# Optimization experiments

Measured on AMD Instinct MI355X. Metric: run time of the kernel, lower is better.

Reference implementation:

```python
import jax, jax.numpy as jnp
import numpy as np

HEADS = 4
KS = 7          # neighborhood kernel size
EPS = 1e-5
C = 64
N, H, W = 8, 64, 64


def _gather_idx(L, k):
    # NATTEN-style neighborhood: window centered at pixel, shifted to stay in bounds.
    start = jnp.clip(jnp.arange(L) - k // 2, 0, L - k)            # [L]
    idx = start[:, None] + jnp.arange(k)                           # [L, k] absolute neighbor idx
    # relative-position-bias index: (query - neighbor) + (k-1) in [0, 2k-2]
    rel = (jnp.arange(L) - start)[:, None] + (k - 1) - jnp.arange(k)[None, :]  # [L, k]
    return idx, rel


def na2d(x, qkv_w, qkv_b, rpb, proj_w, proj_b):
    # x: [N, H, W, C] -> neighborhood attention with rel-pos bias
    n, h, w, c = x.shape
    hd = c // HEADS
    scale = hd ** -0.5
    qkv = (x @ qkv_w.T + qkv_b).reshape(n, h, w, 3, HEADS, hd)
    q = qkv[..., 0, :, :] * scale                                  # [n,h,w,heads,hd]
    k = qkv[..., 1, :, :]
    v = qkv[..., 2, :, :]
    idx_h, rel_h = _gather_idx(h, KS)
    idx_w, rel_w = _gather_idx(w, KS)
    # gather neighborhoods: [n, h, k, w, k, heads, hd]
    kg = k[:, idx_h][:, :, :, idx_w]
    vg = v[:, idx_h][:, :, :, idx_w]
    attn = jnp.einsum('nijhd,niajbhd->nijhab', q, kg)              # [n,h,w,heads,k,k]
    bias = rpb[:, rel_h, :]                                        # [heads, h, k, 2k-1]
    bias = jnp.take(bias, rel_w, axis=-1)                          # [heads, h, k, w, k]
    bias = jnp.transpose(bias, (1, 3, 0, 2, 4))                    # [h, w, heads, k, k]
    attn = attn + bias
    a = jax.nn.softmax(attn.reshape(n, h, w, HEADS, KS * KS), axis=-1).reshape(attn.shape)
    out = jnp.einsum('nijhab,niajbhd->nijhd', a, vg).reshape(n, h, w, c)
    return out @ proj_w.T + proj_b


def setup_inputs() -> dict:
    key = jax.random.key(0)
    ks = jax.random.split(key, 12)
    s = 0.02
    return {
        'x': jax.random.normal(ks[0], (N, C, H, W), jnp.float32),
        'gn_w': jnp.ones((C,), jnp.float32),
        'gn_b': jnp.zeros((C,), jnp.float32),
        'qkv_w': jax.random.normal(ks[1], (3 * C, C), jnp.float32) * s,
        'qkv_b': jnp.zeros((3 * C,), jnp.float32),
        'rpb': jax.random.normal(ks[2], (HEADS, 2 * KS - 1, 2 * KS - 1), jnp.float32) * s,
        'proj_w': jax.random.normal(ks[3], (C, C), jnp.float32) * s,
        'proj_b': jnp.zeros((C,), jnp.float32),
        'ln_w': jnp.ones((C,), jnp.float32),
        'ln_b': jnp.zeros((C,), jnp.float32),
        'fc1_w': jax.random.normal(ks[4], (4 * C, C), jnp.float32) * s,
        'fc1_b': jnp.zeros((4 * C,), jnp.float32),
        'fc2_w': jax.random.normal(ks[5], (C, 4 * C), jnp.float32) * s,
        'fc2_b': jnp.zeros((C,), jnp.float32),
    }


def reference(x, gn_w, gn_b, qkv_w, qkv_b, rpb, proj_w, proj_b,
              ln_w, ln_b, fc1_w, fc1_b, fc2_w, fc2_b):
    n, c, h, w = x.shape
    x1 = jnp.transpose(x, (0, 2, 3, 1))                            # residual, NHWC
    # GroupNorm(1, C): normalize over (C,H,W) per sample, per-channel affine
    mu = jnp.mean(x, axis=(1, 2, 3), keepdims=True)
    var = jnp.var(x, axis=(1, 2, 3), keepdims=True)
    xg = (x - mu) * jax.lax.rsqrt(var + EPS)
    xg = xg * gn_w[None, :, None, None] + gn_b[None, :, None, None]
    xg = jnp.transpose(xg, (0, 2, 3, 1))                           # NHWC
    y = na2d(xg, qkv_w, qkv_b, rpb, proj_w, proj_b) + x1           # [n,h,w,c]
    y = y.reshape(n, h * w, c)
    # LayerNorm over channels + MLP (GELU), residual
    mu2 = jnp.mean(y, axis=-1, keepdims=True)
    var2 = jnp.var(y, axis=-1, keepdims=True)
    yn = (y - mu2) * jax.lax.rsqrt(var2 + EPS) * ln_w + ln_b
    hdn = jax.nn.gelu(yn @ fc1_w.T + fc1_b, approximate=False)
    y = y + (hdn @ fc2_w.T + fc2_b)
    return jnp.transpose(y.reshape(n, h, w, c), (0, 3, 1, 2))      # back to NCHW
```

## Files before the change

### kernel.cpp

```cpp
#include <hip/hip_runtime.h>
#include <math.h>

#define NSAMP 8
#define CH 64
#define HH 64
#define WW 64
#define SPATIAL 4096
#define PER_SAMPLE 262144
#define NTOK 32768
#define NHEADS 4
#define HD 16
#define KS 7
#define EPS 1e-5f
#define QSCALE 0.25f

typedef __attribute__((ext_vector_type(8))) short short8;
typedef __attribute__((ext_vector_type(4))) float f32x4;

__device__ __forceinline__ unsigned short f2bf(float f) {
    unsigned u = __float_as_uint(f);
    u = u + 0x7fffu + ((u >> 16) & 1u);
    return (unsigned short)(u >> 16);
}
__device__ __forceinline__ unsigned pack2(float a, float b) {
    return (unsigned)f2bf(a) | ((unsigned)f2bf(b) << 16);
}
__device__ __forceinline__ float dot8_bf(uint4 u, const float* qv) {
    float s;
    s = __uint_as_float(u.x << 16) * qv[0];
    s = fmaf(__uint_as_float(u.x & 0xffff0000u), qv[1], s);
    s = fmaf(__uint_as_float(u.y << 16),         qv[2], s);
    s = fmaf(__uint_as_float(u.y & 0xffff0000u), qv[3], s);
    s = fmaf(__uint_as_float(u.z << 16),         qv[4], s);
    s = fmaf(__uint_as_float(u.z & 0xffff0000u), qv[5], s);
    s = fmaf(__uint_as_float(u.w << 16),         qv[6], s);
    s = fmaf(__uint_as_float(u.w & 0xffff0000u), qv[7], s);
    return s;
}
__device__ __forceinline__ void pv8_bf(uint4 u, float p, float* acc) {
    acc[0] = fmaf(p, __uint_as_float(u.x << 16),         acc[0]);
    acc[1] = fmaf(p, __uint_as_float(u.x & 0xffff0000u), acc[1]);
    acc[2] = fmaf(p, __uint_as_float(u.y << 16),         acc[2]);
    acc[3] = fmaf(p, __uint_as_float(u.y & 0xffff0000u), acc[3]);
    acc[4] = fmaf(p, __uint_as_float(u.z << 16),         acc[4]);
    acc[5] = fmaf(p, __uint_as_float(u.z & 0xffff0000u), acc[5]);
    acc[6] = fmaf(p, __uint_as_float(u.w << 16),         acc[6]);
    acc[7] = fmaf(p, __uint_as_float(u.w & 0xffff0000u), acc[7]);
}

__global__ __launch_bounds__(256) void k_prep(const float* __restrict__ qkv_w,
                                              const float* __restrict__ fc1_w,
                                              const float* __restrict__ fc2_w,
                                              const float* __restrict__ proj_w,
                                              unsigned short* __restrict__ wb) {
    int i = blockIdx.x * 256 + threadIdx.x;
    if (i < 12288)      wb[i] = f2bf(qkv_w[i]);
    else if (i < 28672) wb[i] = f2bf(fc1_w[i - 12288]);
    else if (i < 45056) wb[i] = f2bf(fc2_w[i - 28672]);
    else if (i < 49152) wb[i] = f2bf(proj_w[i - 45056]);
}

__global__ __launch_bounds__(256) void k_stats(const float* __restrict__ x,
                                               float* __restrict__ stats) {
    int blk = blockIdx.x;
    int n = blk >> 5, chunk = blk & 31;
    const float4* p4 = (const float4*)(x + n * PER_SAMPLE + chunk * 8192);
    int t = threadIdx.x;
    float s1 = 0.f, s2 = 0.f;
#pragma unroll
    for (int i = 0; i < 8; i++) {
        float4 v = p4[t + i * 256];
        s1 += v.x + v.y + v.z + v.w;
        s2 += v.x * v.x + v.y * v.y + v.z * v.z + v.w * v.w;
    }
#pragma unroll
    for (int off = 1; off < 64; off <<= 1) {
        s1 += __shfl_xor(s1, off);
        s2 += __shfl_xor(s2, off);
    }
    __shared__ float r1[4], r2[4];
    int lane = t & 63, wv = t >> 6;
    if (lane == 0) { r1[wv] = s1; r2[wv] = s2; }
    __syncthreads();
    if (t == 0) {
        atomicAdd(&stats[n * 2 + 0], r1[0] + r1[1] + r1[2] + r1[3]);
        atomicAdd(&stats[n * 2 + 1], r2[0] + r2[1] + r2[2] + r2[3]);
    }
}

__global__ __launch_bounds__(256) void k_qkv(const float* __restrict__ x,
                                             const float* __restrict__ stats,
                                             const float* __restrict__ gn_w,
                                             const float* __restrict__ gn_b,
                                             const unsigned short* __restrict__ qkv_wb,
                                             const float* __restrict__ qkv_b,
                                             uint4* __restrict__ qb8,
                                             uint4* __restrict__ kvb8) {
    __shared__ __attribute__((aligned(16))) short xA[4 * 2 * 64 * 8];
    __shared__ float obuf[4][16 * 65];
    int s0 = blockIdx.x * 64;
    int smp = s0 >> 12, sp = s0 & 4095;
    int t = threadIdx.x, tok = t & 63, g = t >> 6;

    float mu = stats[2 * smp] * (1.f / (float)PER_SAMPLE);
    float var = stats[2 * smp + 1] * (1.f / (float)PER_SAMPLE) - mu * mu;
    float rstd = rsqrtf(var + EPS);

    {
        const float* xp = x + smp * PER_SAMPLE + sp + tok;
        float v[16];
#pragma unroll
        for (int i = 0; i < 16; i++) {
            int c = g * 16 + i;
            v[i] = (xp[(size_t)c * SPATIAL] - mu) * rstd * gn_w[c] + gn_b[c];
        }
#pragma unroll
        for (int e = 0; e < 2; e++) {
            int cb = 2 * g + e;
            int kf = cb >> 2, qq = cb & 3;
            uint4 p;
            p.x = pack2(v[e * 8 + 0], v[e * 8 + 1]);
            p.y = pack2(v[e * 8 + 2], v[e * 8 + 3]);
            p.z = pack2(v[e * 8 + 4], v[e * 8 + 5]);
            p.w = pack2(v[e * 8 + 6], v[e * 8 + 7]);
            int chunk = ((tok >> 4) * 2 + kf) * 64 + (tok & 15) + (qq << 4);
            *(uint4*)&xA[chunk * 8] = p;
        }
    }
    __syncthreads();

    int w = __builtin_amdgcn_readfirstlane(g);
    int lane = t & 63, nh = lane & 15, qd = lane >> 4;

    short8 af[8];
#pragma unroll
    for (int mt = 0; mt < 4; mt++)
#pragma unroll
        for (int kf = 0; kf < 2; kf++)
            af[mt * 2 + kf] = *(const short8*)&xA[((mt * 2 + kf) * 64 + lane) * 8];

    for (int nt = 0; nt < 3; nt++) {
        int n0 = w * 48 + nt * 16;
        const unsigned short* wp = qkv_wb + (size_t)(n0 + nh) * 64 + qd * 8;
        short8 b0 = *(const short8*)(wp);
        short8 b1 = *(const short8*)(wp + 32);
        float bias = qkv_b[n0 + nh];
        bool isq = (n0 < 64);
        f32x4 acc[4];
#pragma unroll
        for (int mt = 0; mt < 4; mt++) {
            f32x4 d = {0.f, 0.f, 0.f, 0.f};
            d = __builtin_amdgcn_mfma_f32_16x16x32_bf16(af[mt * 2 + 0], b0, d, 0, 0, 0);
            d = __builtin_amdgcn_mfma_f32_16x16x32_bf16(af[mt * 2 + 1], b1, d, 0, 0, 0);
            acc[mt] = d;
        }
#pragma unroll
        for (int mt = 0; mt < 4; mt++)
#pragma unroll
            for (int r = 0; r < 4; r++) {
                float vv = acc[mt][r] + bias;
                if (isq) vv *= QSCALE;
                obuf[w][nh * 65 + mt * 16 + qd * 4 + r] = vv;
            }
        __syncthreads();
#pragma unroll
        for (int u = 0; u < 2; u++) {
            uint4 p;
            p.x = pack2(obuf[w][(u * 8 + 0) * 65 + lane], obuf[w][(u * 8 + 1) * 65 + lane]);
            p.y = pack2(obuf[w][(u * 8 + 2) * 65 + lane], obuf[w][(u * 8 + 3) * 65 + lane]);
            p.z = pack2(obuf[w][(u * 8 + 4) * 65 + lane], obuf[w][(u * 8 + 5) * 65 + lane]);
            p.w = pack2(obuf[w][(u * 8 + 6) * 65 + lane], obuf[w][(u * 8 + 7) * 65 + lane]);
            if (n0 < 64)
                qb8[(size_t)((n0 >> 3) + u) * NTOK + s0 + lane] = p;
            else if (n0 < 128)
                kvb8[(size_t)(((n0 - 64) >> 3) + u) * NTOK + s0 + lane] = p;
            else
                kvb8[(size_t)(8 + ((n0 - 128) >> 3) + u) * NTOK + s0 + lane] = p;
        }
        __syncthreads();
    }
}

__global__ __launch_bounds__(256) void k_attnproj(const uint4* __restrict__ qb8,
                                                  const uint4* __restrict__ kvb8,
                                                  const float* __restrict__ rpb,
                                                  const unsigned short* __restrict__ proj_wb,
                                                  const float* __restrict__ proj_b,
                                                  const float* __restrict__ x,
                                                  float4* __restrict__ y4) {
    __shared__ __attribute__((aligned(16))) short xA[4 * 2 * 64 * 8];
    __shared__ float obuf[4][16 * 65];
    int b = blockIdx.x;
    int n = b >> 6, h = b & 63;
    int t = threadIdx.x, w = t & 63;
    int head = __builtin_amdgcn_readfirstlane(t >> 6);
    int rowbase = n * 4096 + h * 64;

    float q[16];
    {
        uint4 qa = qb8[(size_t)(2 * head) * NTOK + rowbase + w];
        uint4 qc = qb8[(size_t)(2 * head + 1) * NTOK + rowbase + w];
        q[0] = __uint_as_float(qa.x << 16); q[1] = __uint_as_float(qa.x & 0xffff0000u);
        q[2] = __uint_as_float(qa.y << 16); q[3] = __uint_as_float(qa.y & 0xffff0000u);
        q[4] = __uint_as_float(qa.z << 16); q[5] = __uint_as_float(qa.z & 0xffff0000u);
        q[6] = __uint_as_float(qa.w << 16); q[7] = __uint_as_float(qa.w & 0xffff0000u);
        q[8]  = __uint_as_float(qc.x << 16); q[9]  = __uint_as_float(qc.x & 0xffff0000u);
        q[10] = __uint_as_float(qc.y << 16); q[11] = __uint_as_float(qc.y & 0xffff0000u);
        q[12] = __uint_as_float(qc.z << 16); q[13] = __uint_as_float(qc.z & 0xffff0000u);
        q[14] = __uint_as_float(qc.w << 16); q[15] = __uint_as_float(qc.w & 0xffff0000u);
    }
    int sh = min(max(h - 3, 0), HH - KS);
    int sw = min(max(w - 3, 0), WW - KS);

    float lg[49];
    float mx = -1e30f;
#pragma unroll
    for (int a = 0; a < 7; a++) {
        int nb = n * 4096 + (sh + a) * 64 + sw;
        const float* rp = rpb + (head * 13 + (h - sh + 6 - a)) * 13;
#pragma unroll
        for (int bb = 0; bb < 7; bb++) {
            size_t base = (size_t)(2 * head) * NTOK + nb + bb;
            float d = dot8_bf(kvb8[base], q) + dot8_bf(kvb8[base + NTOK], q + 8);
            d += rp[w - sw + 6 - bb];
            lg[a * 7 + bb] = d;
            mx = fmaxf(mx, d);
        }
    }
    float sum = 0.f;
#pragma unroll
    for (int i = 0; i < 49; i++) {
        float e = __expf(lg[i] - mx);
        lg[i] = e;
        sum += e;
    }
    float rs = 1.f / sum;

    float acc[16];
#pragma unroll
    for (int i = 0; i < 16; i++) acc[i] = 0.f;
#pragma unroll
    for (int a = 0; a < 7; a++) {
        int nb = n * 4096 + (sh + a) * 64 + sw;
#pragma unroll
        for (int bb = 0; bb < 7; bb++) {
            size_t base = (size_t)(8 + 2 * head) * NTOK + nb + bb;
            float p = lg[a * 7 + bb];
            pv8_bf(kvb8[base], p, acc);
            pv8_bf(kvb8[base + NTOK], p, acc + 8);
        }
    }

#pragma unroll
    for (int e = 0; e < 2; e++) {
        int cb = 2 * head + e;
        int kf = cb >> 2, qq = cb & 3;
        uint4 p;
        p.x = pack2(acc[e * 8 + 0] * rs, acc[e * 8 + 1] * rs);
        p.y = pack2(acc[e * 8 + 2] * rs, acc[e * 8 + 3] * rs);
        p.z = pack2(acc[e * 8 + 4] * rs, acc[e * 8 + 5] * rs);
        p.w = pack2(acc[e * 8 + 6] * rs, acc[e * 8 + 7] * rs);
        int chunk = ((w >> 4) * 2 + kf) * 64 + (w & 15) + (qq << 4);
        *(uint4*)&xA[chunk * 8] = p;
    }
    __syncthreads();

    int lane = t & 63, nh = lane & 15, qd = lane >> 4;
    short8 af[8];
#pragma unroll
    for (int mt = 0; mt < 4; mt++)
#pragma unroll
        for (int kf = 0; kf < 2; kf++)
            af[mt * 2 + kf] = *(const short8*)&xA[((mt * 2 + kf) * 64 + lane) * 8];

    int n0 = head * 16;
    const unsigned short* wp = proj_wb + (size_t)(n0 + nh) * 64 + qd * 8;
    short8 b0 = *(const short8*)(wp);
    short8 b1 = *(const short8*)(wp + 32);
    float bias = proj_b[n0 + nh];
#pragma unroll
    for (int mt = 0; mt < 4; mt++) {
        f32x4 d = {0.f, 0.f, 0.f, 0.f};
        d = __builtin_amdgcn_mfma_f32_16x16x32_bf16(af[mt * 2 + 0], b0, d, 0, 0, 0);
        d = __builtin_amdgcn_mfma_f32_16x16x32_bf16(af[mt * 2 + 1], b1, d, 0, 0, 0);
#pragma unroll
        for (int r = 0; r < 4; r++)
            obuf[head][nh * 65 + mt * 16 + qd * 4 + r] = d[r] + bias;
    }
    __syncthreads();

    const float* xr = x + n * PER_SAMPLE + h * 64;
#pragma unroll
    for (int u = 0; u < 4; u++) {
        int cg = (n0 >> 2) + u;
        float4 o;
        o.x = obuf[head][(u * 4 + 0) * 65 + lane] + xr[(size_t)(cg * 4 + 0) * SPATIAL + lane];
        o.y = obuf[head][(u * 4 + 1) * 65 + lane] + xr[(size_t)(cg * 4 + 1) * SPATIAL + lane];
        o.z = obuf[head][(u * 4 + 2) * 65 + lane] + xr[(size_t)(cg * 4 + 2) * SPATIAL + lane];
        o.w = obuf[head][(u * 4 + 3) * 65 + lane] + xr[(size_t)(cg * 4 + 3) * SPATIAL + lane];
        y4[(size_t)cg * NTOK + rowbase + lane] = o;
    }
}

__global__ __launch_bounds__(256) void k_mlp(const float4* __restrict__ y4,
                                             const float* __restrict__ ln_w,
                                             const float* __restrict__ ln_b,
                                             const unsigned short* __restrict__ fc1_wb,
                                             const float* __restrict__ fc1_b,
                                             const unsigned short* __restrict__ fc2_wb,
                                             const float* __restrict__ fc2_b,
                                             float* __restrict__ out) {
    __shared__ __attribute__((aligned(16))) short ynA[4 * 2 * 64 * 8];
    __shared__ __attribute__((aligned(16))) short lhA[4 * 8 * 64 * 8];
    __shared__ float obuf[4][16 * 65];
    __shared__ float red1[256], red2[256];
    int s0 = blockIdx.x * 64;
    int smp = s0 >> 12, sp = s0 & 4095;
    int t = threadIdx.x, tok = t & 63, g = t >> 6;

    float v[16];
    float s1 = 0.f, s2 = 0.f;
#pragma unroll
    for (int i = 0; i < 4; i++) {
        float4 yy = y4[(size_t)(g * 4 + i) * NTOK + s0 + tok];
        v[i * 4 + 0] = yy.x; v[i * 4 + 1] = yy.y; v[i * 4 + 2] = yy.z; v[i * 4 + 3] = yy.w;
        s1 += yy.x + yy.y + yy.z + yy.w;
        s2 += yy.x * yy.x + yy.y * yy.y + yy.z * yy.z + yy.w * yy.w;
    }
    red1[g * 64 + tok] = s1;
    red2[g * 64 + tok] = s2;
    __syncthreads();
    float mu = (red1[tok] + red1[64 + tok] + red1[128 + tok] + red1[192 + tok]) * (1.f / 64.f);
    float sq = (red2[tok] + red2[64 + tok] + red2[128 + tok] + red2[192 + tok]) * (1.f / 64.f);
    float rstd = rsqrtf(sq - mu * mu + EPS);
#pragma unroll
    for (int i = 0; i < 16; i++) {
        int c = g * 16 + i;
        v[i] = (v[i] - mu) * rstd * ln_w[c] + ln_b[c];
    }
#pragma unroll
    for (int e = 0; e < 2; e++) {
        int cb = 2 * g + e;
        int kf = cb >> 2, qq = cb & 3;
        uint4 p;
        p.x = pack2(v[e * 8 + 0], v[e * 8 + 1]);
        p.y = pack2(v[e * 8 + 2], v[e * 8 + 3]);
        p.z = pack2(v[e * 8 + 4], v[e * 8 + 5]);
        p.w = pack2(v[e * 8 + 6], v[e * 8 + 7]);
        int chunk = ((tok >> 4) * 2 + kf) * 64 + (tok & 15) + (qq << 4);
        *(uint4*)&ynA[chunk * 8] = p;
    }
    __syncthreads();

    int w = __builtin_amdgcn_readfirstlane(g);
    int lane = t & 63, nh = lane & 15, q = lane >> 4;

    {
        short8 af[8];
#pragma unroll
        for (int mt = 0; mt < 4; mt++)
#pragma unroll
            for (int kf = 0; kf < 2; kf++)
                af[mt * 2 + kf] = *(const short8*)&ynA[((mt * 2 + kf) * 64 + lane) * 8];

        for (int nt = 0; nt < 4; nt++) {
            int n0 = w * 64 + nt * 16;
            const unsigned short* wp = fc1_wb + (size_t)(n0 + nh) * 64 + q * 8;
            short8 b0 = *(const short8*)(wp);
            short8 b1 = *(const short8*)(wp + 32);
            float bias = fc1_b[n0 + nh];
            int j = n0 + nh;
            int kf2 = j >> 5, q2 = (j >> 3) & 3, jb = j & 7;
#pragma unroll
            for (int mt = 0; mt < 4; mt++) {
                f32x4 d = {0.f, 0.f, 0.f, 0.f};
                d = __builtin_amdgcn_mfma_f32_16x16x32_bf16(af[mt * 2 + 0], b0, d, 0, 0, 0);
                d = __builtin_amdgcn_mfma_f32_16x16x32_bf16(af[mt * 2 + 1], b1, d, 0, 0, 0);
#pragma unroll
                for (int r = 0; r < 4; r++) {
                    float hv = d[r] + bias;
                    hv = 0.5f * hv * (1.f + erff(hv * 0.70710678118654752f));
                    lhA[(mt * 8 + kf2) * 512 + ((q * 4 + r) + (q2 << 4)) * 8 + jb] = (short)f2bf(hv);
                }
            }
        }
    }
    __syncthreads();

    {
        int n0 = w * 16;
        f32x4 acc[4];
#pragma unroll
        for (int mt = 0; mt < 4; mt++) acc[mt] = (f32x4){0.f, 0.f, 0.f, 0.f};
#pragma unroll
        for (int kf = 0; kf < 8; kf++) {
            const unsigned short* wp = fc2_wb + (size_t)(n0 + nh) * 256 + kf * 32 + q * 8;
            short8 b = *(const short8*)(wp);
#pragma unroll
            for (int mt = 0; mt < 4; mt++) {
                short8 a = *(const short8*)&lhA[((mt * 8 + kf) * 64 + lane) * 8];
                acc[mt] = __builtin_amdgcn_mfma_f32_16x16x32_bf16(a, b, acc[mt], 0, 0, 0);
            }
        }
#pragma unroll
        for (int mt = 0; mt < 4; mt++)
#pragma unroll
            for (int r = 0; r < 4; r++)
                obuf[w][nh * 65 + mt * 16 + q * 4 + r] = acc[mt][r];
        __syncthreads();

        float* op = out + (size_t)smp * PER_SAMPLE + sp;
#pragma unroll
        for (int u = 0; u < 4; u++) {
            int cg = (n0 >> 2) + u;
            float4 res = y4[(size_t)cg * NTOK + s0 + lane];
            float rr[4] = {res.x, res.y, res.z, res.w};
#pragma unroll
            for (int e = 0; e < 4; e++) {
                int c = cg * 4 + e;
                op[(size_t)c * SPATIAL + lane] = obuf[w][(u * 4 + e) * 65 + lane] + fc2_b[c] + rr[e];
            }
        }
    }
}

extern "C" void kernel_launch(void* const* d_in, const int* in_sizes, int n_in,
                              void* d_out, int out_size, void* d_ws, size_t ws_size,
                              hipStream_t stream) {
    const float* x      = (const float*)d_in[0];
    const float* gn_w   = (const float*)d_in[1];
    const float* gn_b   = (const float*)d_in[2];
    const float* qkv_w  = (const float*)d_in[3];
    const float* qkv_b  = (const float*)d_in[4];
    const float* rpb    = (const float*)d_in[5];
    const float* proj_w = (const float*)d_in[6];
    const float* proj_b = (const float*)d_in[7];
    const float* ln_w   = (const float*)d_in[8];
    const float* ln_b   = (const float*)d_in[9];
    const float* fc1_w  = (const float*)d_in[10];
    const float* fc1_b  = (const float*)d_in[11];
    const float* fc2_w  = (const float*)d_in[12];
    const float* fc2_b  = (const float*)d_in[13];
    float* out = (float*)d_out;

    float* ws    = (float*)d_ws;
    float* stats = ws;
    uint4* qb8   = (uint4*)(ws + 64);
    uint4* kvb8  = qb8 + (size_t)8 * NTOK;
    float4* y4   = (float4*)(kvb8 + (size_t)16 * NTOK);
    unsigned short* wb = (unsigned short*)(y4 + (size_t)16 * NTOK);
    unsigned short* qkv_wb  = wb;
    unsigned short* fc1_wb  = wb + 12288;
    unsigned short* fc2_wb  = wb + 28672;
    unsigned short* proj_wb = wb + 45056;

    hipMemsetAsync(stats, 0, 64, stream);
    k_prep    <<<192, 256, 0, stream>>>(qkv_w, fc1_w, fc2_w, proj_w, wb);
    k_stats   <<<256, 256, 0, stream>>>(x, stats);
    k_qkv     <<<512, 256, 0, stream>>>(x, stats, gn_w, gn_b, qkv_wb, qkv_b, qb8, kvb8);
    k_attnproj<<<512, 256, 0, stream>>>(qb8, kvb8, rpb, proj_wb, proj_b, x, y4);
    k_mlp     <<<512, 256, 0, stream>>>(y4, ln_w, ln_b, fc1_wb, fc1_b, fc2_wb, fc2_b, out);
}
```

Baseline: 137.5 us.

## Fuse attention-proj with MLP kernel and merge weight prep into stats

Merges the attention+projection kernel with the LayerNorm+MLP kernel so the residual activations stay in shared memory (ybuf) instead of being written to and re-read from a global y4 buffer. The MLP hidden layer is processed in two halves to shrink the lhA shared buffer. Weight bf16 conversion is folded into the stats kernel as extra blocks, removing one launch. Block-wide barriers in k_qkv around per-wave obuf use are replaced with wave barriers. Shared memory per block grows, which may reduce occupancy.

```diff
diff --git a/kernel.cpp b/kernel.cpp
--- a/kernel.cpp
+++ b/kernel.cpp
@@ -48,21 +48,22 @@
     acc[7] = fmaf(p, __uint_as_float(u.w & 0xffff0000u), acc[7]);
 }
 
-__global__ __launch_bounds__(256) void k_prep(const float* __restrict__ qkv_w,
-                                              const float* __restrict__ fc1_w,
-                                              const float* __restrict__ fc2_w,
-                                              const float* __restrict__ proj_w,
-                                              unsigned short* __restrict__ wb) {
-    int i = blockIdx.x * 256 + threadIdx.x;
-    if (i < 12288)      wb[i] = f2bf(qkv_w[i]);
-    else if (i < 28672) wb[i] = f2bf(fc1_w[i - 12288]);
-    else if (i < 45056) wb[i] = f2bf(fc2_w[i - 28672]);
-    else if (i < 49152) wb[i] = f2bf(proj_w[i - 45056]);
-}
-
-__global__ __launch_bounds__(256) void k_stats(const float* __restrict__ x,
-                                               float* __restrict__ stats) {
+__global__ __launch_bounds__(256) void k_statsprep(const float* __restrict__ x,
+                                                   float* __restrict__ stats,
+                                                   const float* __restrict__ qkv_w,
+                                                   const float* __restrict__ fc1_w,
+                                                   const float* __restrict__ fc2_w,
+                                                   const float* __restrict__ proj_w,
+                                                   unsigned short* __restrict__ wb) {
     int blk = blockIdx.x;
+    if (blk >= 256) {
+        int i = (blk - 256) * 256 + threadIdx.x;
+        if (i < 12288)      wb[i] = f2bf(qkv_w[i]);
+        else if (i < 28672) wb[i] = f2bf(fc1_w[i - 12288]);
+        else if (i < 45056) wb[i] = f2bf(fc2_w[i - 28672]);
+        else                wb[i] = f2bf(proj_w[i - 45056]);
+        return;
+    }
     int n = blk >> 5, chunk = blk & 31;
     const float4* p4 = (const float4*)(x + n * PER_SAMPLE + chunk * 8192);
     int t = threadIdx.x;
@@ -162,7 +163,7 @@
                 if (isq) vv *= QSCALE;
                 obuf[w][nh * 65 + mt * 16 + qd * 4 + r] = vv;
             }
-        __syncthreads();
+        __builtin_amdgcn_wave_barrier();
 #pragma unroll
         for (int u = 0; u < 2; u++) {
             uint4 p;
@@ -177,29 +178,37 @@
             else
                 kvb8[(size_t)(8 + ((n0 - 128) >> 3) + u) * NTOK + s0 + lane] = p;
         }
-        __syncthreads();
-    }
-}
-
-__global__ __launch_bounds__(256) void k_attnproj(const uint4* __restrict__ qb8,
-                                                  const uint4* __restrict__ kvb8,
-                                                  const float* __restrict__ rpb,
-                                                  const unsigned short* __restrict__ proj_wb,
-                                                  const float* __restrict__ proj_b,
-                                                  const float* __restrict__ x,
-                                                  float4* __restrict__ y4) {
-    __shared__ __attribute__((aligned(16))) short xA[4 * 2 * 64 * 8];
+        __builtin_amdgcn_wave_barrier();
+    }
+}
+
+__global__ __launch_bounds__(256) void k_fused(const uint4* __restrict__ qb8,
+                                               const uint4* __restrict__ kvb8,
+                                               const float* __restrict__ rpb,
+                                               const unsigned short* __restrict__ proj_wb,
+                                               const float* __restrict__ proj_b,
+                                               const float* __restrict__ x,
+                                               const float* __restrict__ ln_w,
+                                               const float* __restrict__ ln_b,
+                                               const unsigned short* __restrict__ fc1_wb,
+                                               const float* __restrict__ fc1_b,
+                                               const unsigned short* __restrict__ fc2_wb,
+                                               const float* __restrict__ fc2_b,
+                                               float* __restrict__ out) {
+    __shared__ __attribute__((aligned(16))) short fragA[4 * 2 * 64 * 8];
+    __shared__ __attribute__((aligned(16))) short lhA[4 * 4 * 64 * 8];
     __shared__ float obuf[4][16 * 65];
-    int b = blockIdx.x;
-    int n = b >> 6, h = b & 63;
+    __shared__ float ybuf[64 * 65];
+    __shared__ float red1[256], red2[256];
+    int b = blockIdx.x, n = b >> 6, h = b & 63;
     int t = threadIdx.x, w = t & 63;
-    int head = __builtin_amdgcn_readfirstlane(t >> 6);
+    int g = __builtin_amdgcn_readfirstlane(t >> 6);
     int rowbase = n * 4096 + h * 64;
 
     float q[16];
     {
-        uint4 qa = qb8[(size_t)(2 * head) * NTOK + rowbase + w];
-        uint4 qc = qb8[(size_t)(2 * head + 1) * NTOK + rowbase + w];
+        uint4 qa = qb8[(size_t)(2 * g) * NTOK + rowbase + w];
+        uint4 qc = qb8[(size_t)(2 * g + 1) * NTOK + rowbase + w];
         q[0] = __uint_as_float(qa.x << 16); q[1] = __uint_as_float(qa.x & 0xffff0000u);
         q[2] = __uint_as_float(qa.y << 16); q[3] = __uint_as_float(qa.y & 0xffff0000u);
         q[4] = __uint_as_float(qa.z << 16); q[5] = __uint_as_float(qa.z & 0xffff0000u);
@@ -217,10 +226,10 @@
 #pragma unroll
     for (int a = 0; a < 7; a++) {
         int nb = n * 4096 + (sh + a) * 64 + sw;
-        const float* rp = rpb + (head * 13 + (h - sh + 6 - a)) * 13;
+        const float* rp = rpb + (g * 13 + (h - sh + 6 - a)) * 13;
 #pragma unroll
         for (int bb = 0; bb < 7; bb++) {
-            size_t base = (size_t)(2 * head) * NTOK + nb + bb;
+            size_t base = (size_t)(2 * g) * NTOK + nb + bb;
             float d = dot8_bf(kvb8[base], q) + dot8_bf(kvb8[base + NTOK], q + 8);
             d += rp[w - sw + 6 - bb];
             lg[a * 7 + bb] = d;
@@ -244,16 +253,15 @@
         int nb = n * 4096 + (sh + a) * 64 + sw;
 #pragma unroll
         for (int bb = 0; bb < 7; bb++) {
-            size_t base = (size_t)(8 + 2 * head) * NTOK + nb + bb;
+            size_t base = (size_t)(8 + 2 * g) * NTOK + nb + bb;
             float p = lg[a * 7 + bb];
             pv8_bf(kvb8[base], p, acc);
             pv8_bf(kvb8[base + NTOK], p, acc + 8);
         }
     }
-
 #pragma unroll
     for (int e = 0; e < 2; e++) {
-        int cb = 2 * head + e;
+        int cb = 2 * g + e;
         int kf = cb >> 2, qq = cb & 3;
         uint4 p;
         p.x = pack2(acc[e * 8 + 0] * rs, acc[e * 8 + 1] * rs);
@@ -261,165 +269,145 @@
         p.z = pack2(acc[e * 8 + 4] * rs, acc[e * 8 + 5] * rs);
         p.w = pack2(acc[e * 8 + 6] * rs, acc[e * 8 + 7] * rs);
         int chunk = ((w >> 4) * 2 + kf) * 64 + (w & 15) + (qq << 4);
-        *(uint4*)&xA[chunk * 8] = p;
+        *(uint4*)&fragA[chunk * 8] = p;
     }
     __syncthreads();
 
     int lane = t & 63, nh = lane & 15, qd = lane >> 4;
-    short8 af[8];
-#pragma unroll
-    for (int mt = 0; mt < 4; mt++)
-#pragma unroll
-        for (int kf = 0; kf < 2; kf++)
-            af[mt * 2 + kf] = *(const short8*)&xA[((mt * 2 + kf) * 64 + lane) * 8];
-
-    int n0 = head * 16;
-    const unsigned short* wp = proj_wb + (size_t)(n0 + nh) * 64 + qd * 8;
-    short8 b0 = *(const short8*)(wp);
-    short8 b1 = *(const short8*)(wp + 32);
-    float bias = proj_b[n0 + nh];
-#pragma unroll
-    for (int mt = 0; mt < 4; mt++) {
-        f32x4 d = {0.f, 0.f, 0.f, 0.f};
-        d = __builtin_amdgcn_mfma_f32_16x16x32_bf16(af[mt * 2 + 0], b0, d, 0, 0, 0);
-        d = __builtin_amdgcn_mfma_f32_16x16x32_bf16(af[mt * 2 + 1], b1, d, 0, 0, 0);
-#pragma unroll
-        for (int r = 0; r < 4; r++)
-            obuf[head][nh * 65 + mt * 16 + qd * 4 + r] = d[r] + bias;
-    }
-    __syncthreads();
-
-    const float* xr = x + n * PER_SAMPLE + h * 64;
-#pragma unroll
-    for (int u = 0; u < 4; u++) {
-        int cg = (n0 >> 2) + u;
-        float4 o;
-        o.x = obuf[head][(u * 4 + 0) * 65 + lane] + xr[(size_t)(cg * 4 + 0) * SPATIAL + lane];
-        o.y = obuf[head][(u * 4 + 1) * 65 + lane] + xr[(size_t)(cg * 4 + 1) * SPATIAL + lane];
-        o.z = obuf[head][(u * 4 + 2) * 65 + lane] + xr[(size_t)(cg * 4 + 2) * SPATIAL + lane];
-        o.w = obuf[head][(u * 4 + 3) * 65 + lane] + xr[(size_t)(cg * 4 + 3) * SPATIAL + lane];
-        y4[(size_t)cg * NTOK + rowbase + lane] = o;
-    }
-}
-
-__global__ __launch_bounds__(256) void k_mlp(const float4* __restrict__ y4,
-                                             const float* __restrict__ ln_w,
-                                             const float* __restrict__ ln_b,
-                                             const unsigned short* __restrict__ fc1_wb,
-                                             const float* __restrict__ fc1_b,
-                                             const unsigned short* __restrict__ fc2_wb,
-                                             const float* __restrict__ fc2_b,
-                                             float* __restrict__ out) {
-    __shared__ __attribute__((aligned(16))) short ynA[4 * 2 * 64 * 8];
-    __shared__ __attribute__((aligned(16))) short lhA[4 * 8 * 64 * 8];
-    __shared__ float obuf[4][16 * 65];
-    __shared__ float red1[256], red2[256];
-    int s0 = blockIdx.x * 64;
-    int smp = s0 >> 12, sp = s0 & 4095;
-    int t = threadIdx.x, tok = t & 63, g = t >> 6;
-
-    float v[16];
-    float s1 = 0.f, s2 = 0.f;
-#pragma unroll
-    for (int i = 0; i < 4; i++) {
-        float4 yy = y4[(size_t)(g * 4 + i) * NTOK + s0 + tok];
-        v[i * 4 + 0] = yy.x; v[i * 4 + 1] = yy.y; v[i * 4 + 2] = yy.z; v[i * 4 + 3] = yy.w;
-        s1 += yy.x + yy.y + yy.z + yy.w;
-        s2 += yy.x * yy.x + yy.y * yy.y + yy.z * yy.z + yy.w * yy.w;
-    }
-    red1[g * 64 + tok] = s1;
-    red2[g * 64 + tok] = s2;
-    __syncthreads();
-    float mu = (red1[tok] + red1[64 + tok] + red1[128 + tok] + red1[192 + tok]) * (1.f / 64.f);
-    float sq = (red2[tok] + red2[64 + tok] + red2[128 + tok] + red2[192 + tok]) * (1.f / 64.f);
-    float rstd = rsqrtf(sq - mu * mu + EPS);
-#pragma unroll
-    for (int i = 0; i < 16; i++) {
-        int c = g * 16 + i;
-        v[i] = (v[i] - mu) * rstd * ln_w[c] + ln_b[c];
-    }
-#pragma unroll
-    for (int e = 0; e < 2; e++) {
-        int cb = 2 * g + e;
-        int kf = cb >> 2, qq = cb & 3;
-        uint4 p;
-        p.x = pack2(v[e * 8 + 0], v[e * 8 + 1]);
-        p.y = pack2(v[e * 8 + 2], v[e * 8 + 3]);
-        p.z = pack2(v[e * 8 + 4], v[e * 8 + 5]);
-        p.w = pack2(v[e * 8 + 6], v[e * 8 + 7]);
-        int chunk = ((tok >> 4) * 2 + kf) * 64 + (tok & 15) + (qq << 4);
-        *(uint4*)&ynA[chunk * 8] = p;
-    }
-    __syncthreads();
-
-    int w = __builtin_amdgcn_readfirstlane(g);
-    int lane = t & 63, nh = lane & 15, q = lane >> 4;
-
     {
         short8 af[8];
 #pragma unroll
         for (int mt = 0; mt < 4; mt++)
 #pragma unroll
             for (int kf = 0; kf < 2; kf++)
-                af[mt * 2 + kf] = *(const short8*)&ynA[((mt * 2 + kf) * 64 + lane) * 8];
-
-        for (int nt = 0; nt < 4; nt++) {
-            int n0 = w * 64 + nt * 16;
-            const unsigned short* wp = fc1_wb + (size_t)(n0 + nh) * 64 + q * 8;
+                af[mt * 2 + kf] = *(const short8*)&fragA[((mt * 2 + kf) * 64 + lane) * 8];
+
+        int n0 = g * 16;
+        const unsigned short* wp = proj_wb + (size_t)(n0 + nh) * 64 + qd * 8;
+        short8 b0 = *(const short8*)(wp);
+        short8 b1 = *(const short8*)(wp + 32);
+        float bias = proj_b[n0 + nh];
+#pragma unroll
+        for (int mt = 0; mt < 4; mt++) {
+            f32x4 d = {0.f, 0.f, 0.f, 0.f};
+            d = __builtin_amdgcn_mfma_f32_16x16x32_bf16(af[mt * 2 + 0], b0, d, 0, 0, 0);
+            d = __builtin_amdgcn_mfma_f32_16x16x32_bf16(af[mt * 2 + 1], b1, d, 0, 0, 0);
+#pragma unroll
+            for (int r = 0; r < 4; r++)
+                obuf[g][nh * 65 + mt * 16 + qd * 4 + r] = d[r] + bias;
+        }
+        __builtin_amdgcn_wave_barrier();
+        const float* xr = x + n * PER_SAMPLE + h * 64;
+#pragma unroll
+        for (int u = 0; u < 4; u++) {
+#pragma unroll
+            for (int e = 0; e < 4; e++) {
+                int c = g * 16 + u * 4 + e;
+                ybuf[c * 65 + lane] = obuf[g][(u * 4 + e) * 65 + lane]
+                                    + xr[(size_t)c * SPATIAL + lane];
+            }
+        }
+    }
+    __syncthreads();
+
+    {
+        float v[16];
+        float s1 = 0.f, s2 = 0.f;
+#pragma unroll
+        for (int i = 0; i < 16; i++) {
+            float vv = ybuf[(g * 16 + i) * 65 + w];
+            v[i] = vv; s1 += vv; s2 += vv * vv;
+        }
+        red1[g * 64 + w] = s1;
+        red2[g * 64 + w] = s2;
+        __syncthreads();
+        float mu = (red1[w] + red1[64 + w] + red1[128 + w] + red1[192 + w]) * (1.f / 64.f);
+        float sq = (red2[w] + red2[64 + w] + red2[128 + w] + red2[192 + w]) * (1.f / 64.f);
+        float rstd = rsqrtf(sq - mu * mu + EPS);
+#pragma unroll
+        for (int i = 0; i < 16; i++) {
+            int c = g * 16 + i;
+            v[i] = (v[i] - mu) * rstd * ln_w[c] + ln_b[c];
+        }
+#pragma unroll
+        for (int e = 0; e < 2; e++) {
+            int cb = 2 * g + e;
+            int kf = cb >> 2, qq = cb & 3;
+            uint4 p;
+            p.x = pack2(v[e * 8 + 0], v[e * 8 + 1]);
+            p.y = pack2(v[e * 8 + 2], v[e * 8 + 3]);
+            p.z = pack2(v[e * 8 + 4], v[e * 8 + 5]);
+            p.w = pack2(v[e * 8 + 6], v[e * 8 + 7]);
+            int chunk = ((w >> 4) * 2 + kf) * 64 + (w & 15) + (qq << 4);
+            *(uint4*)&fragA[chunk * 8] = p;
+        }
+    }
+    __syncthreads();
+
+    short8 yf[8];
+#pragma unroll
+    for (int mt = 0; mt < 4; mt++)
+#pragma unroll
+        for (int kf = 0; kf < 2; kf++)
+            yf[mt * 2 + kf] = *(const short8*)&fragA[((mt * 2 + kf) * 64 + lane) * 8];
+
+    f32x4 acc2[4];
+#pragma unroll
+    for (int mt = 0; mt < 4; mt++) acc2[mt] = (f32x4){0.f, 0.f, 0.f, 0.f};
+
+    for (int half = 0; half < 2; half++) {
+#pragma unroll
+        for (int nt = 0; nt < 2; nt++) {
+            int n0f = half * 128 + g * 32 + nt * 16;
+            const unsigned short* wp = fc1_wb + (size_t)(n0f + nh) * 64 + qd * 8;
             short8 b0 = *(const short8*)(wp);
             short8 b1 = *(const short8*)(wp + 32);
-            float bias = fc1_b[n0 + nh];
-            int j = n0 + nh;
-            int kf2 = j >> 5, q2 = (j >> 3) & 3, jb = j & 7;
+            float bias = fc1_b[n0f + nh];
+            int j = n0f + nh;
+            int kfl = (j - half * 128) >> 5;
+            int q2 = (j >> 3) & 3, jb = j & 7;
 #pragma unroll
             for (int mt = 0; mt < 4; mt++) {
                 f32x4 d = {0.f, 0.f, 0.f, 0.f};
-                d = __builtin_amdgcn_mfma_f32_16x16x32_bf16(af[mt * 2 + 0], b0, d, 0, 0, 0);
-                d = __builtin_amdgcn_mfma_f32_16x16x32_bf16(af[mt * 2 + 1], b1, d, 0, 0, 0);
+                d = __builtin_amdgcn_mfma_f32_16x16x32_bf16(yf[mt * 2 + 0], b0, d, 0, 0, 0);
+                d = __builtin_amdgcn_mfma_f32_16x16x32_bf16(yf[mt * 2 + 1], b1, d, 0, 0, 0);
 #pragma unroll
                 for (int r = 0; r < 4; r++) {
                     float hv = d[r] + bias;
                     hv = 0.5f * hv * (1.f + erff(hv * 0.70710678118654752f));
-                    lhA[(mt * 8 + kf2) * 512 + ((q * 4 + r) + (q2 << 4)) * 8 + jb] = (short)f2bf(hv);
+                    lhA[(mt * 4 + kfl) * 512 + ((qd * 4 + r) + (q2 << 4)) * 8 + jb] = (short)f2bf(hv);
                 }
             }
         }
-    }
-    __syncthreads();
-
-    {
-        int n0 = w * 16;
-        f32x4 acc[4];
-#pragma unroll
-        for (int mt = 0; mt < 4; mt++) acc[mt] = (f32x4){0.f, 0.f, 0.f, 0.f};
-#pragma unroll
-        for (int kf = 0; kf < 8; kf++) {
-            const unsigned short* wp = fc2_wb + (size_t)(n0 + nh) * 256 + kf * 32 + q * 8;
-            short8 b = *(const short8*)(wp);
+        __syncthreads();
+#pragma unroll
+        for (int kf = 0; kf < 4; kf++) {
+            int kfg = half * 4 + kf;
+            const unsigned short* wp = fc2_wb + (size_t)(g * 16 + nh) * 256 + kfg * 32 + qd * 8;
+            short8 bb = *(const short8*)(wp);
 #pragma unroll
             for (int mt = 0; mt < 4; mt++) {
-                short8 a = *(const short8*)&lhA[((mt * 8 + kf) * 64 + lane) * 8];
-                acc[mt] = __builtin_amdgcn_mfma_f32_16x16x32_bf16(a, b, acc[mt], 0, 0, 0);
+                short8 a = *(const short8*)&lhA[((mt * 4 + kf) * 64 + lane) * 8];
+                acc2[mt] = __builtin_amdgcn_mfma_f32_16x16x32_bf16(a, bb, acc2[mt], 0, 0, 0);
             }
         }
-#pragma unroll
-        for (int mt = 0; mt < 4; mt++)
-#pragma unroll
-            for (int r = 0; r < 4; r++)
-                obuf[w][nh * 65 + mt * 16 + q * 4 + r] = acc[mt][r];
         __syncthreads();
-
-        float* op = out + (size_t)smp * PER_SAMPLE + sp;
-#pragma unroll
-        for (int u = 0; u < 4; u++) {
-            int cg = (n0 >> 2) + u;
-            float4 res = y4[(size_t)cg * NTOK + s0 + lane];
-            float rr[4] = {res.x, res.y, res.z, res.w};
-#pragma unroll
-            for (int e = 0; e < 4; e++) {
-                int c = cg * 4 + e;
-                op[(size_t)c * SPATIAL + lane] = obuf[w][(u * 4 + e) * 65 + lane] + fc2_b[c] + rr[e];
-            }
+    }
+
+#pragma unroll
+    for (int mt = 0; mt < 4; mt++)
+#pragma unroll
+        for (int r = 0; r < 4; r++)
+            obuf[g][nh * 65 + mt * 16 + qd * 4 + r] = acc2[mt][r];
+    __builtin_amdgcn_wave_barrier();
+    float* op = out + (size_t)n * PER_SAMPLE + h * 64;
+#pragma unroll
+    for (int u = 0; u < 4; u++) {
+#pragma unroll
+        for (int e = 0; e < 4; e++) {
+            int c = g * 16 + u * 4 + e;
+            op[(size_t)c * SPATIAL + lane] = obuf[g][(u * 4 + e) * 65 + lane]
+                                           + fc2_b[c] + ybuf[c * 65 + lane];
         }
     }
 }
@@ -447,17 +435,15 @@
     float* stats = ws;
     uint4* qb8   = (uint4*)(ws + 64);
     uint4* kvb8  = qb8 + (size_t)8 * NTOK;
-    float4* y4   = (float4*)(kvb8 + (size_t)16 * NTOK);
-    unsigned short* wb = (unsigned short*)(y4 + (size_t)16 * NTOK);
+    unsigned short* wb = (unsigned short*)(kvb8 + (size_t)16 * NTOK);
     unsigned short* qkv_wb  = wb;
     unsigned short* fc1_wb  = wb + 12288;
     unsigned short* fc2_wb  = wb + 28672;
     unsigned short* proj_wb = wb + 45056;
 
     hipMemsetAsync(stats, 0, 64, stream);
-    k_prep    <<<192, 256, 0, stream>>>(qkv_w, fc1_w, fc2_w, proj_w, wb);
-    k_stats   <<<256, 256, 0, stream>>>(x, stats);
-    k_qkv     <<<512, 256, 0, stream>>>(x, stats, gn_w, gn_b, qkv_wb, qkv_b, qb8, kvb8);
-    k_attnproj<<<512, 256, 0, stream>>>(qb8, kvb8, rpb, proj_wb, proj_b, x, y4);
-    k_mlp     <<<512, 256, 0, stream>>>(y4, ln_w, ln_b, fc1_wb, fc1_b, fc2_wb, fc2_b, out);
-}
+    k_statsprep<<<448, 256, 0, stream>>>(x, stats, qkv_w, fc1_w, fc2_w, proj_w, wb);
+    k_qkv      <<<512, 256, 0, stream>>>(x, stats, gn_w, gn_b, qkv_wb, qkv_b, qb8, kvb8);
+    k_fused    <<<512, 256, 0, stream>>>(qb8, kvb8, rpb, proj_wb, proj_b, x,
+                                         ln_w, ln_b, fc1_wb, fc1_b, fc2_wb, fc2_b, out);
+}
```

Result: faster. 132.0 us (-4.0%).
